# Kernel optimization log

Hardware: AMD Instinct MI355X
Metric: run time of the kernel (lower is better)

Reference implementation:

```python
import jax, jax.numpy as jnp
import numpy as np

ALPHA = 0.25
GAMMA = 2.0
VAR0, VAR1 = 0.1, 0.2  # torch.Tensor([0.1, 0.2]) variances in encode
EPS = 1e-4


def _center_size(boxes):
    # corner (x1,y1,x2,y2) -> center (cx,cy,w,h)
    return jnp.concatenate([(boxes[:, :2] + boxes[:, 2:]) * 0.5,
                            boxes[:, 2:] - boxes[:, :2]], axis=1)


def _jaccard(a, b):
    # a: [A,4] anchors, b: [T,4] targets, corner form -> IoU [A,T]
    lt = jnp.maximum(a[:, None, :2], b[None, :, :2])
    rb = jnp.minimum(a[:, None, 2:], b[None, :, 2:])
    wh = jnp.clip(rb - lt, 0.0)
    inter = wh[..., 0] * wh[..., 1]
    area_a = (a[:, 2] - a[:, 0]) * (a[:, 3] - a[:, 1])
    area_b = (b[:, 2] - b[:, 0]) * (b[:, 3] - b[:, 1])
    return inter / (area_a[:, None] + area_b[None, :] - inter)


def _encode(matched, priors_cf):
    # matched: corner form [P,4]; priors_cf: center form [P,4]
    g_cxcy = ((matched[:, :2] + matched[:, 2:]) * 0.5 - priors_cf[:, :2]) / (VAR0 * priors_cf[:, 2:])
    g_wh = jnp.log((matched[:, 2:] - matched[:, :2]) / priors_cf[:, 2:]) / VAR1
    return jnp.concatenate([g_cxcy, g_wh], axis=1)


def _per_image(cla, reg, target, anchor, anchor_cf):
    # cla [A,C], reg [A,4], target [T,5]
    valid = target[:, 4] != -1.0                      # padded targets (label -1) are excluded
    has_valid = jnp.any(valid)
    cla = jnp.clip(cla, EPS, 1.0 - EPS)
    iou = _jaccard(anchor, target[:, :4])             # [A,T]
    iou = jnp.where(valid[None, :], iou, -1.0)        # mask padded targets (valid IoUs are >= 0)
    iou_argmax = jnp.argmax(iou, axis=1)              # [A]
    iou_max = jnp.take_along_axis(iou, iou_argmax[:, None], axis=1)[:, 0]
    pos = iou_max >= 0.5
    num_pos = jnp.sum(pos)
    assigned = target[iou_argmax]                     # [A,5] gather of matched gt

    C = cla.shape[1]
    onehot = jax.nn.one_hot(assigned[:, 4].astype(jnp.int32), C, dtype=cla.dtype)
    labels = jnp.full_like(cla, -1.0)
    labels = jnp.where(iou_max[:, None] < 0.4, 0.0, labels)
    labels = jnp.where(pos[:, None], onehot, labels)

    is_one = labels == 1.0
    alpha_factor = jnp.where(is_one, ALPHA, 1.0 - ALPHA)
    focal_weight = alpha_factor * jnp.where(is_one, 1.0 - cla, cla) ** GAMMA
    bce = -(labels * jnp.log(cla) + (1.0 - labels) * jnp.log1p(-cla))
    cls_loss = jnp.where(labels != -1.0, focal_weight * bce, 0.0)
    cls_loss = cls_loss.sum() / jnp.maximum(num_pos.astype(cla.dtype), 1.0)

    # smooth-L1 on positive anchors only; original takes .mean() over [P,4]
    enc_gt = _encode(assigned[:, :4], anchor_cf)      # [A,4]
    diff = jnp.abs(enc_gt - reg)
    sl1 = jnp.where(diff <= 1.0 / 9.0, 0.5 * 9.0 * diff * diff, diff - 0.5 / 9.0)
    denom = jnp.maximum(num_pos * 4, 1).astype(cla.dtype)
    reg_loss = jnp.where(num_pos > 0, jnp.sum(sl1 * pos[:, None]) / denom, 0.0)

    cls_loss = jnp.where(has_valid, cls_loss, 0.0)
    reg_loss = jnp.where(has_valid, reg_loss, 0.0)
    return cls_loss, reg_loss


def setup_inputs() -> dict:
    key = jax.random.key(0)
    ks = jax.random.split(key, 7)
    B, A, C, T = 8, 100000, 80, 50
    clas = jax.random.uniform(ks[0], (B, A, C), jnp.float32, 0.01, 0.99)
    regs = jax.random.normal(ks[1], (B, A, 4), jnp.float32)
    # anchors: valid corner boxes inside a ~1024x1024 image
    axy = jax.random.uniform(ks[2], (1, A, 2), jnp.float32, 0.0, 900.0)
    awh = jax.random.uniform(ks[3], (1, A, 2), jnp.float32, 16.0, 120.0)
    anchors = jnp.concatenate([axy, axy + awh], axis=-1)
    # targets: valid gt boxes with class id in [0, C) stored as float in column 4
    txy = jax.random.uniform(ks[4], (B, T, 2), jnp.float32, 0.0, 800.0)
    twh = jax.random.uniform(ks[5], (B, T, 2), jnp.float32, 20.0, 220.0)
    lab = jax.random.randint(ks[6], (B, T, 1), 0, C).astype(jnp.float32)
    targets = jnp.concatenate([txy, txy + twh, lab], axis=-1)
    return {"clas": clas, "regs": regs, "anchors": anchors, "targets": targets}


def reference(clas, regs, anchors, targets):
    anchor = anchors[0]                               # [A,4]
    anchor_cf = _center_size(anchor)
    cls_l, reg_l = jax.vmap(_per_image, in_axes=(0, 0, 0, None, None))(
        clas, regs, targets, anchor, anchor_cf)
    return (jnp.mean(cls_l, keepdims=True), jnp.mean(reg_l, keepdims=True))
```

## Files before the change

### kernel.cpp

```cpp
#include <hip/hip_runtime.h>

#define A_COUNT 100000
#define B_COUNT 8
#define C_COUNT 80
#define T_COUNT 50
#define BLOCK   256
#define NF4     (C_COUNT / 4)
#define FULL4   (BLOCK * NF4)

typedef float f4v __attribute__((ext_vector_type(4)));

__global__ __launch_bounds__(BLOCK) void retina_main(
    const float* __restrict__ clas,
    const float* __restrict__ regs,
    const float* __restrict__ anchors,
    const float* __restrict__ targets,
    float* __restrict__ ws_cls,
    float* __restrict__ ws_reg,
    int*   __restrict__ ws_pos)
{
    __shared__ float s_tgt[T_COUNT * 5];
    __shared__ int   s_state[BLOCK];
    __shared__ float s_c[4], s_r[4];
    __shared__ int   s_p[4];

    const int b    = blockIdx.y;
    const int base = blockIdx.x * BLOCK;
    const int tid  = threadIdx.x;

    for (int i = tid; i < T_COUNT * 5; i += BLOCK)
        s_tgt[i] = targets[b * T_COUNT * 5 + i];
    __syncthreads();

    const int a = base + tid;
    int   state  = -1;
    float my_reg = 0.0f;
    bool  my_pos = false;

    if (a < A_COUNT) {
        const float4 an = ((const float4*)anchors)[a];
        const float area_a = (an.z - an.x) * (an.w - an.y);

        float best = -1.0f;
        int   bestIdx = 0;
        bool  anyValid = false;

        #pragma unroll 1
        for (int t = 0; t < T_COUNT; ++t) {
            const float tx1 = s_tgt[t * 5 + 0];
            const float ty1 = s_tgt[t * 5 + 1];
            const float tx2 = s_tgt[t * 5 + 2];
            const float ty2 = s_tgt[t * 5 + 3];
            const float lab = s_tgt[t * 5 + 4];
            float iou = -1.0f;
            if (lab != -1.0f) {
                anyValid = true;
                const float lx = fmaxf(an.x, tx1), ly = fmaxf(an.y, ty1);
                const float rx = fminf(an.z, tx2), ry = fminf(an.w, ty2);
                const float w = fmaxf(rx - lx, 0.0f);
                const float h = fmaxf(ry - ly, 0.0f);
                const float inter  = w * h;
                const float area_b = (tx2 - tx1) * (ty2 - ty1);
                iou = inter / (area_a + area_b - inter);
            }
            if (iou > best) { best = iou; bestIdx = t; }
        }

        if (anyValid) {
            if (best >= 0.5f) {
                state  = (int)s_tgt[bestIdx * 5 + 4];
                my_pos = true;
                const float4 rg = ((const float4*)regs)[(size_t)b * A_COUNT + a];
                const float tx1 = s_tgt[bestIdx * 5 + 0];
                const float ty1 = s_tgt[bestIdx * 5 + 1];
                const float tx2 = s_tgt[bestIdx * 5 + 2];
                const float ty2 = s_tgt[bestIdx * 5 + 3];
                const float pcx = (an.x + an.z) * 0.5f, pcy = (an.y + an.w) * 0.5f;
                const float pw  = an.z - an.x,          ph  = an.w - an.y;
                const float mcx = (tx1 + tx2) * 0.5f,   mcy = (ty1 + ty2) * 0.5f;
                const float mw  = tx2 - tx1,            mh  = ty2 - ty1;
                const float e0 = (mcx - pcx) / (0.1f * pw);
                const float e1 = (mcy - pcy) / (0.1f * ph);
                const float e2 = __logf(mw / pw) * 5.0f;
                const float e3 = __logf(mh / ph) * 5.0f;
                const float d0 = fabsf(e0 - rg.x);
                const float d1 = fabsf(e1 - rg.y);
                const float d2 = fabsf(e2 - rg.z);
                const float d3 = fabsf(e3 - rg.w);
                const float th = 1.0f / 9.0f;
                const float c59 = 0.5f / 9.0f;
                const float s0 = (d0 <= th) ? 4.5f * d0 * d0 : d0 - c59;
                const float s1 = (d1 <= th) ? 4.5f * d1 * d1 : d1 - c59;
                const float s2 = (d2 <= th) ? 4.5f * d2 * d2 : d2 - c59;
                const float s3 = (d3 <= th) ? 4.5f * d3 * d3 : d3 - c59;
                my_reg = s0 + s1 + s2 + s3;
            } else if (best < 0.4f) {
                state = 128;
            }
        }
    }
    s_state[tid] = state;
    __syncthreads();

    const int nA = min(BLOCK, A_COUNT - base);
    const f4v* cl4 = (const f4v*)(clas + ((size_t)b * A_COUNT + base) * C_COUNT);
    float cls_local = 0.0f;

    if (nA == BLOCK) {
        int aL = tid / NF4;
        int cL = tid - aL * NF4;
        #pragma unroll
        for (int ko = 0; ko < 5; ++ko) {
            f4v v[4];
            #pragma unroll
            for (int u = 0; u < 4; ++u)
                v[u] = __builtin_nontemporal_load(&cl4[tid + (ko * 4 + u) * BLOCK]);
            #pragma unroll
            for (int u = 0; u < 4; ++u) {
                const int st  = s_state[aL];
                const float w = (st == -1) ? 0.0f : 0.75f;
                #pragma unroll
                for (int j = 0; j < 4; ++j) {
                    float p = fminf(fmaxf(v[u][j], 1e-4f), 1.0f - 1e-4f);
                    float l = __logf(1.0f - p);
                    cls_local = fmaf(p * p * l, -w, cls_local);
                }
                aL += 12; cL += 16;
                if (cL >= NF4) { cL -= NF4; ++aL; }
            }
        }
    } else {
        const int count4 = nA * NF4;
        for (int i = tid; i < count4; i += BLOCK) {
            const int st = s_state[i / NF4];
            if (st == -1) continue;
            const f4v v = __builtin_nontemporal_load(&cl4[i]);
            #pragma unroll
            for (int j = 0; j < 4; ++j) {
                float p = fminf(fmaxf(v[j], 1e-4f), 1.0f - 1e-4f);
                float l = __logf(1.0f - p);
                cls_local = fmaf(p * p * l, -0.75f, cls_local);
            }
        }
    }

    if (my_pos) {
        float p = clas[((size_t)b * A_COUNT + a) * C_COUNT + state];
        p = fminf(fmaxf(p, 1e-4f), 1.0f - 1e-4f);
        const float om = 1.0f - p;
        cls_local += 0.25f * om * om * (-__logf(p))
                   - 0.75f * p * p * (-__logf(om));
    }

    float r0 = cls_local, r1 = my_reg;
    const unsigned long long bal = __ballot(my_pos);
    const int posc = __popcll(bal);
    #pragma unroll
    for (int off = 32; off > 0; off >>= 1) {
        r0 += __shfl_down(r0, off);
        r1 += __shfl_down(r1, off);
    }
    const int wave = tid >> 6, lane = tid & 63;
    if (lane == 0) { s_c[wave] = r0; s_r[wave] = r1; s_p[wave] = posc; }
    __syncthreads();
    if (tid == 0) {
        float tc = 0.0f, tr = 0.0f; int tp = 0;
        #pragma unroll
        for (int w = 0; w < 4; ++w) { tc += s_c[w]; tr += s_r[w]; tp += s_p[w]; }
        atomicAdd(&ws_cls[b], tc);
        atomicAdd(&ws_reg[b], tr);
        atomicAdd(&ws_pos[b], tp);
    }
}

__global__ void retina_final(const float* __restrict__ ws_cls,
                             const float* __restrict__ ws_reg,
                             const int*   __restrict__ ws_pos,
                             float* __restrict__ out)
{
    const int tid = threadIdx.x;
    float cl = 0.0f, rl = 0.0f;
    if (tid < B_COUNT) {
        const int   npi = ws_pos[tid];
        const float np  = (float)npi;
        cl = ws_cls[tid] / fmaxf(np, 1.0f);
        rl = (npi > 0) ? ws_reg[tid] / (np * 4.0f) : 0.0f;
    }
    #pragma unroll
    for (int off = 4; off > 0; off >>= 1) {
        cl += __shfl_down(cl, off);
        rl += __shfl_down(rl, off);
    }
    if (tid == 0) {
        out[0] = cl * (1.0f / (float)B_COUNT);
        out[1] = rl * (1.0f / (float)B_COUNT);
    }
}

extern "C" void kernel_launch(void* const* d_in, const int* in_sizes, int n_in,
                              void* d_out, int out_size, void* d_ws, size_t ws_size,
                              hipStream_t stream) {
    const float* clas    = (const float*)d_in[0];
    const float* regs    = (const float*)d_in[1];
    const float* anchors = (const float*)d_in[2];
    const float* targets = (const float*)d_in[3];

    float* ws_cls = (float*)d_ws;
    float* ws_reg = ws_cls + B_COUNT;
    int*   ws_pos = (int*)(ws_reg + B_COUNT);

    hipMemsetAsync(d_ws, 0, (2 * B_COUNT) * sizeof(float) + B_COUNT * sizeof(int), stream);

    dim3 grid((A_COUNT + BLOCK - 1) / BLOCK, B_COUNT);
    retina_main<<<grid, BLOCK, 0, stream>>>(clas, regs, anchors, targets,
                                            ws_cls, ws_reg, ws_pos);
    retina_final<<<1, 64, 0, stream>>>(ws_cls, ws_reg, ws_pos, (float*)d_out);
}
```

Before: 401.5 us.

## Prefetch first half of class scores before IoU matching loop

Issues nontemporal loads for the first 10 float4 chunks of each block's class-score tile before the 50-target IoU loop, so that memory latency overlaps with the matching compute. The remaining 10 chunks are loaded as one batch after the barrier instead of in groups of four. The anchor load is also hoisted ahead of the loop. This raises register pressure by about 40 live VGPRs across the IoU loop, which could lower occupancy.

Result: no change. 408.7 us (+1.8%).

```diff
diff --git a/kernel.cpp b/kernel.cpp
--- a/kernel.cpp
+++ b/kernel.cpp
@@ -6,7 +6,6 @@
 #define T_COUNT 50
 #define BLOCK   256
 #define NF4     (C_COUNT / 4)
-#define FULL4   (BLOCK * NF4)
 
 typedef float f4v __attribute__((ext_vector_type(4)));
 
@@ -27,18 +26,30 @@
     const int b    = blockIdx.y;
     const int base = blockIdx.x * BLOCK;
     const int tid  = threadIdx.x;
+    const int nA   = min(BLOCK, A_COUNT - base);
+    const bool full = (nA == BLOCK);
+    const int a    = base + tid;
 
     for (int i = tid; i < T_COUNT * 5; i += BLOCK)
         s_tgt[i] = targets[b * T_COUNT * 5 + i];
     __syncthreads();
 
-    const int a = base + tid;
+    float4 an = make_float4(0.f, 0.f, 1.f, 1.f);
+    if (a < A_COUNT) an = ((const float4*)anchors)[a];
+
+    const f4v* cl4 = (const f4v*)(clas + ((size_t)b * A_COUNT + base) * C_COUNT);
+    f4v v0[10];
+    if (full) {
+        #pragma unroll
+        for (int u = 0; u < 10; ++u)
+            v0[u] = __builtin_nontemporal_load(&cl4[tid + u * BLOCK]);
+    }
+
     int   state  = -1;
     float my_reg = 0.0f;
     bool  my_pos = false;
 
     if (a < A_COUNT) {
-        const float4 an = ((const float4*)anchors)[a];
         const float area_a = (an.z - an.x) * (an.w - an.y);
 
         float best = -1.0f;
@@ -87,7 +98,7 @@
                 const float d1 = fabsf(e1 - rg.y);
                 const float d2 = fabsf(e2 - rg.z);
                 const float d3 = fabsf(e3 - rg.w);
-                const float th = 1.0f / 9.0f;
+                const float th  = 1.0f / 9.0f;
                 const float c59 = 0.5f / 9.0f;
                 const float s0 = (d0 <= th) ? 4.5f * d0 * d0 : d0 - c59;
                 const float s1 = (d1 <= th) ? 4.5f * d1 * d1 : d1 - c59;
@@ -102,31 +113,36 @@
     s_state[tid] = state;
     __syncthreads();
 
-    const int nA = min(BLOCK, A_COUNT - base);
-    const f4v* cl4 = (const f4v*)(clas + ((size_t)b * A_COUNT + base) * C_COUNT);
     float cls_local = 0.0f;
 
-    if (nA == BLOCK) {
-        int aL = tid / NF4;
-        int cL = tid - aL * NF4;
-        #pragma unroll
-        for (int ko = 0; ko < 5; ++ko) {
-            f4v v[4];
+    if (full) {
+        f4v v1[10];
+        #pragma unroll
+        for (int u = 0; u < 10; ++u)
+            v1[u] = __builtin_nontemporal_load(&cl4[tid + (10 + u) * BLOCK]);
+
+        #pragma unroll
+        for (int u = 0; u < 10; ++u) {
+            const int i  = tid + u * BLOCK;
+            const int st = s_state[i / NF4];
+            const float w = (st == -1) ? 0.0f : 0.75f;
             #pragma unroll
-            for (int u = 0; u < 4; ++u)
-                v[u] = __builtin_nontemporal_load(&cl4[tid + (ko * 4 + u) * BLOCK]);
+            for (int j = 0; j < 4; ++j) {
+                float p = fminf(fmaxf(v0[u][j], 1e-4f), 1.0f - 1e-4f);
+                float l = __logf(1.0f - p);
+                cls_local = fmaf(p * p * l, -w, cls_local);
+            }
+        }
+        #pragma unroll
+        for (int u = 0; u < 10; ++u) {
+            const int i  = tid + (10 + u) * BLOCK;
+            const int st = s_state[i / NF4];
+            const float w = (st == -1) ? 0.0f : 0.75f;
             #pragma unroll
-            for (int u = 0; u < 4; ++u) {
-                const int st  = s_state[aL];
-                const float w = (st == -1) ? 0.0f : 0.75f;
-                #pragma unroll
-                for (int j = 0; j < 4; ++j) {
-                    float p = fminf(fmaxf(v[u][j], 1e-4f), 1.0f - 1e-4f);
-                    float l = __logf(1.0f - p);
-                    cls_local = fmaf(p * p * l, -w, cls_local);
-                }
-                aL += 12; cL += 16;
-                if (cL >= NF4) { cL -= NF4; ++aL; }
+            for (int j = 0; j < 4; ++j) {
+                float p = fminf(fmaxf(v1[u][j], 1e-4f), 1.0f - 1e-4f);
+                float l = __logf(1.0f - p);
+                cls_local = fmaf(p * p * l, -w, cls_local);
             }
         }
     } else {
```
